# Performance work log

Measured on AMD Instinct MI355X. Metric: run time of the kernel, lower is better.

Reference implementation:

```python
import jax, jax.numpy as jnp
import numpy as np

H, KVH, D, BS, L = 32, 8, 128, 16, 4096
MAX_BLOCKS = L // BS          # 256 blocks per sequence (sink cache capacity)
B = 16
NUM_BLOCKS = B * MAX_BLOCKS   # 4096 total cache blocks
T = MAX_BLOCKS * BS           # 4096 linearized cache slots per sequence
SCALE = 1.0 / np.sqrt(D)


def _rope_cos_sin(pos):
    # neox-style RoPE tables; pos: int array [...]. returns cos/sin [..., D/2]
    inv_freq = 1.0 / (10000.0 ** (jnp.arange(0, D, 2, dtype=jnp.float32) / D))
    ang = pos[..., None].astype(jnp.float32) * inv_freq
    return jnp.cos(ang), jnp.sin(ang)


def _apply_rope(x, cos, sin):
    # x [..., D]; cos/sin broadcastable to x[..., :D//2]
    x1, x2 = jnp.split(x, 2, axis=-1)
    return jnp.concatenate([x1 * cos - x2 * sin, x2 * cos + x1 * sin], axis=-1)


def setup_inputs() -> dict:
    key = jax.random.key(0)
    ks = jax.random.split(key, 6)
    q = jax.random.normal(ks[0], (B, H * D), dtype=jnp.float32)
    k = jax.random.normal(ks[1], (B, KVH * D), dtype=jnp.float32)
    v = jax.random.normal(ks[2], (B, KVH * D), dtype=jnp.float32)
    key_cache = jax.random.normal(ks[3], (NUM_BLOCKS, BS, KVH, D), dtype=jnp.float32)
    value_cache = jax.random.normal(ks[4], (NUM_BLOCKS, BS, KVH, D), dtype=jnp.float32)
    block_tables = jnp.arange(B * MAX_BLOCKS, dtype=jnp.int32).reshape(B, MAX_BLOCKS)
    context_lens = jax.random.randint(ks[5], (B,), 0, 6000, dtype=jnp.int32)
    return {"q": q, "k": k, "v": v, "key_cache": key_cache,
            "value_cache": value_cache, "block_tables": block_tables,
            "context_lens": context_lens}


def reference(q, k, v, key_cache, value_cache, block_tables, context_lens):
    ctx = context_lens.astype(jnp.int32)                         # [B] past tokens
    rem = ctx % BS
    # sink/rolling cap: if past >= model_context_len, effective seq len caps
    seq_len = jnp.where(ctx >= L, L - BS + rem + 1, ctx + 1)     # [B]
    pos_q = seq_len - 1                                          # capped current position

    # gather pre-rope keys/values from paged cache -> [B, T, KVH, D]
    keys = key_cache[block_tables].reshape(B, T, KVH, D)
    vals = value_cache[block_tables].reshape(B, T, KVH, D)

    # re-apply rope to gathered keys at their cache-relative positions 0..T-1
    cos_k, sin_k = _rope_cos_sin(jnp.arange(T))                  # [T, D/2]
    keys = _apply_rope(keys, cos_k[None, :, None, :], sin_k[None, :, None, :])

    # rope current q, k at capped positions
    cos_q, sin_q = _rope_cos_sin(pos_q)                          # [B, D/2]
    qh = _apply_rope(q.reshape(B, H, D), cos_q[:, None, :], sin_q[:, None, :])
    kh = _apply_rope(k.reshape(B, KVH, D), cos_q[:, None, :], sin_q[:, None, :])

    # scatter current token's k/v at its slot (offset rem in last used block == seq_len-1)
    bidx = jnp.arange(B)
    keys = keys.at[bidx, pos_q].set(kh)
    vals = vals.at[bidx, pos_q].set(v.reshape(B, KVH, D))

    # GQA attention over first seq_len cached tokens
    G = H // KVH
    qg = qh.reshape(B, KVH, G, D)
    scores = jnp.einsum('bhgd,bthd->bhgt', qg, keys) * SCALE     # [B, KVH, G, T]
    mask = jnp.arange(T)[None, :] < seq_len[:, None]             # [B, T]
    scores = jnp.where(mask[:, None, None, :], scores, jnp.finfo(scores.dtype).min)
    probs = jax.nn.softmax(scores, axis=-1)
    out = jnp.einsum('bhgt,bthd->bhgd', probs, vals)             # [B, KVH, G, D]
    return out.reshape(B, H * D)
```

## Files before the change

kernel.cpp:

```cpp
#include <hip/hip_runtime.h>
#include <math.h>

#define B_      16
#define H_      32
#define KVH_    8
#define G_      4
#define D_      128
#define BS_     16
#define L_      4096
#define MAXB_   256
#define T_      4096
#define NPART_  16
#define PART_   256
#define SCALE_  0.08838834764831843f

__device__ __forceinline__ int seq_len_of(int ctx) {
  return (ctx >= L_) ? (L_ - BS_ + (ctx & (BS_ - 1)) + 1) : (ctx + 1);
}

__global__ void rope_table_kernel(float* __restrict__ tab) {
  int idx = blockIdx.x * blockDim.x + threadIdx.x;
  if (idx >= T_ * 64) return;
  int t = idx >> 6, i = idx & 63;
  double inv = pow(10000.0, -(double)(2 * i) / 128.0);
  float ang = (float)t * (float)inv;
  double a = (double)ang;
  tab[2 * idx]     = (float)cos(a);
  tab[2 * idx + 1] = (float)sin(a);
}


#define LOADK(P, tt)                                                        \
  {                                                                         \
    int blk_  = sblk[((tt) - t0) >> 4];                                     \
    int base_ = ((blk_ * BS_ + ((tt) & (BS_ - 1))) * KVH_ + kvh) * D_;      \
    const float4* kc4_ = (const float4*)(kc + base_);                       \
    const float4* vc4_ = (const float4*)(vc + base_);                       \
    P##ka = kc4_[dg];      P##kb = kc4_[16 + dg];                           \
    P##va = vc4_[dg];      P##vb = vc4_[16 + dg];                           \
    P##c0 = tab4[(tt) * 32 + 2 * dg];                                       \
    P##c1 = tab4[(tt) * 32 + 2 * dg + 1];                                   \
  }

#define COMPUTE(P, tt)                                                      \
  {                                                                         \
    float kr1[4], kr2[4];                                                   \
    kr1[0] = P##ka.x * P##c0.x - P##kb.x * P##c0.y;                         \
    kr2[0] = P##kb.x * P##c0.x + P##ka.x * P##c0.y;                         \
    kr1[1] = P##ka.y * P##c0.z - P##kb.y * P##c0.w;                         \
    kr2[1] = P##kb.y * P##c0.z + P##ka.y * P##c0.w;                         \
    kr1[2] = P##ka.z * P##c1.x - P##kb.z * P##c1.y;                         \
    kr2[2] = P##kb.z * P##c1.x + P##ka.z * P##c1.y;                         \
    kr1[3] = P##ka.w * P##c1.z - P##kb.w * P##c1.w;                         \
    kr2[3] = P##kb.w * P##c1.z + P##ka.w * P##c1.w;                         \
    float4 va_ = P##va, vb_ = P##vb;                                        \
    if ((tt) == posq) {         \
      const float* kp_ = knew + b * (KVH_ * D_) + kvh * D_;                 \
      float4 a_  = *(const float4*)(kp_ + 4 * dg);                          \
      float4 b_  = *(const float4*)(kp_ + 64 + 4 * dg);                     \
      float4 q0_ = tab4[posq * 32 + 2 * dg];                                \
      float4 q1_ = tab4[posq * 32 + 2 * dg + 1];                            \
      kr1[0] = a_.x * q0_.x - b_.x * q0_.y;                                 \
      kr2[0] = b_.x * q0_.x + a_.x * q0_.y;                                 \
      kr1[1] = a_.y * q0_.z - b_.y * q0_.w;                                 \
      kr2[1] = b_.y * q0_.z + a_.y * q0_.w;                                 \
      kr1[2] = a_.z * q1_.x - b_.z * q1_.y;                                 \
      kr2[2] = b_.z * q1_.x + a_.z * q1_.y;                                 \
      kr1[3] = a_.w * q1_.z - b_.w * q1_.w;                                 \
      kr2[3] = b_.w * q1_.z + a_.w * q1_.w;                                 \
      const float* vp_ = vnew + b * (KVH_ * D_) + kvh * D_;                 \
      va_ = *(const float4*)(vp_ + 4 * dg);                                 \
      vb_ = *(const float4*)(vp_ + 64 + 4 * dg);                            \
    }                                                                       \
    float s[G_];                                                            \
    _Pragma("unroll")                                                       \
    for (int g = 0; g < G_; ++g) {                                          \
      s[g] = kr1[0] * q1[g][0] + kr2[0] * q2[g][0]                          \
           + kr1[1] * q1[g][1] + kr2[1] * q2[g][1]                          \
           + kr1[2] * q1[g][2] + kr2[2] * q2[g][2]                          \
           + kr1[3] * q1[g][3] + kr2[3] * q2[g][3];                         \
    }                                                                       \
    _Pragma("unroll")                                                       \
    for (int off = 1; off <= 8; off <<= 1) {                                \
      _Pragma("unroll")                                                     \
      for (int g = 0; g < G_; ++g) s[g] += __shfl_xor(s[g], off);           \
    }                                                                       \
    _Pragma("unroll")                                                       \
    for (int g = 0; g < G_; ++g) {                                          \
      float sv = s[g];                                                      \
      float p;                                                              \
      if (sv > m[g]) {                                                      \
        float corr = __expf(m[g] - sv);                                     \
        l[g] *= corr;                                                       \
        _Pragma("unroll")                                                   \
        for (int j = 0; j < 8; ++j) acc[g][j] *= corr;                      \
        m[g] = sv;                                                          \
        p = 1.0f;                                                           \
      } else {                                                              \
        p = __expf(sv - m[g]);                                              \
      }                                                                     \
      l[g] += p;                                                            \
      acc[g][0] += p * va_.x; acc[g][1] += p * va_.y;                       \
      acc[g][2] += p * va_.z; acc[g][3] += p * va_.w;                       \
      acc[g][4] += p * vb_.x; acc[g][5] += p * vb_.y;                       \
      acc[g][6] += p * vb_.z; acc[g][7] += p * vb_.w;                       \
    }                                                                       \
  }

__global__ __launch_bounds__(256) void attn_partial_kernel(
    const float* __restrict__ q, const float* __restrict__ knew,
    const float* __restrict__ vnew, const float* __restrict__ kc,
    const float* __restrict__ vc, const int* __restrict__ btab,
    const int* __restrict__ ctxl, const float* __restrict__ tab,
    float* __restrict__ opart, float2* __restrict__ ml) {
  int bid  = blockIdx.x;
  int part = bid & (NPART_ - 1);
  int kvh  = (bid >> 4) & (KVH_ - 1);
  int b    = bid >> 7;

  int seq = seq_len_of(ctxl[b]);
  int t0 = part * PART_;
  if (t0 >= seq) return;
  int t1 = min(t0 + PART_, seq);
  int posq = seq - 1;

  int lane = threadIdx.x & 63;
  int wave = threadIdx.x >> 6;
  int tsub = lane >> 4;
  int dg   = lane & 15;

  __shared__ int sblk[PART_ / BS_];
  if (threadIdx.x < PART_ / BS_)
    sblk[threadIdx.x] = btab[b * MAXB_ + (t0 >> 4) + threadIdx.x];
  __syncthreads();

  const float4* tab4 = (const float4*)tab;

  float q1[G_][4], q2[G_][4];
  {
    float4 cq0 = tab4[posq * 32 + 2 * dg];
    float4 cq1 = tab4[posq * 32 + 2 * dg + 1];
#pragma unroll
    for (int g = 0; g < G_; ++g) {
      const float* qp = q + b * (H_ * D_) + (kvh * G_ + g) * D_;
      float4 a  = *(const float4*)(qp + 4 * dg);
      float4 bq = *(const float4*)(qp + 64 + 4 * dg);
      q1[g][0] = (a.x * cq0.x - bq.x * cq0.y) * SCALE_;
      q2[g][0] = (bq.x * cq0.x + a.x * cq0.y) * SCALE_;
      q1[g][1] = (a.y * cq0.z - bq.y * cq0.w) * SCALE_;
      q2[g][1] = (bq.y * cq0.z + a.y * cq0.w) * SCALE_;
      q1[g][2] = (a.z * cq1.x - bq.z * cq1.y) * SCALE_;
      q2[g][2] = (bq.z * cq1.x + a.z * cq1.y) * SCALE_;
      q1[g][3] = (a.w * cq1.z - bq.w * cq1.w) * SCALE_;
      q2[g][3] = (bq.w * cq1.z + a.w * cq1.w) * SCALE_;
    }
  }

  float m[G_], l[G_], acc[G_][8];
#pragma unroll
  for (int g = 0; g < G_; ++g) {
    m[g] = -1e30f; l[g] = 0.f;
#pragma unroll
    for (int j = 0; j < 8; ++j) acc[g][j] = 0.f;
  }

  {
    float4 Aka, Akb, Ava, Avb, Ac0, Ac1;
    float4 Bka, Bkb, Bva, Bvb, Bc0, Bc1;
    int t = t0 + 4 * wave + tsub;
    if (t < t1) {
      LOADK(A, t);
      while (1) {
        int t2 = t + 16;
        if (t2 < t1) LOADK(B, t2);
        COMPUTE(A, t);
        t = t2;
        if (t >= t1) break;
        t2 = t + 16;
        if (t2 < t1) LOADK(A, t2);
        COMPUTE(B, t);
        t = t2;
        if (t >= t1) break;
      }
    }
  }

  auto merge_off = [&](int off) {
#pragma unroll
    for (int g = 0; g < G_; ++g) {
      float mo = __shfl_xor(m[g], off);
      float lo = __shfl_xor(l[g], off);
      float M  = fmaxf(m[g], mo);
      float fa = __expf(m[g] - M);
      float fb = __expf(mo - M);
      l[g] = l[g] * fa + lo * fb;
      m[g] = M;
#pragma unroll
      for (int j = 0; j < 8; ++j) {
        float ao = __shfl_xor(acc[g][j], off);
        acc[g][j] = acc[g][j] * fa + ao * fb;
      }
    }
  };
  merge_off(16);
  merge_off(32);

  __shared__ float  lds_acc[4][G_][D_];
  __shared__ float2 lds_ml[4][G_];
  if (lane < 16) {
#pragma unroll
    for (int g = 0; g < G_; ++g) {
#pragma unroll
      for (int j = 0; j < 8; ++j) {
        int dim = (j < 4) ? (4 * dg + j) : (64 + 4 * dg + (j - 4));
        lds_acc[wave][g][dim] = acc[g][j];
      }
      if (lane == 0) lds_ml[wave][g] = make_float2(m[g], l[g]);
    }
  }
  __syncthreads();
  if (wave == 0) {
    int w = tsub;
#pragma unroll
    for (int g = 0; g < G_; ++g) {
      float2 t2 = lds_ml[w][g];
      m[g] = t2.x; l[g] = t2.y;
#pragma unroll
      for (int j = 0; j < 8; ++j) {
        int dim = (j < 4) ? (4 * dg + j) : (64 + 4 * dg + (j - 4));
        acc[g][j] = lds_acc[w][g][dim];
      }
    }
    merge_off(16);
    merge_off(32);
    if (lane < 16) {
#pragma unroll
      for (int g = 0; g < G_; ++g) {
        float* op = opart + (size_t)(bid * G_ + g) * D_;
#pragma unroll
        for (int j = 0; j < 8; ++j) {
          int dim = (j < 4) ? (4 * dg + j) : (64 + 4 * dg + (j - 4));
          op[dim] = acc[g][j];
        }
        if (lane == 0) ml[bid * G_ + g] = make_float2(m[g], l[g]);
      }
    }
  }
}

__global__ void attn_reduce_kernel(const float* __restrict__ opart,
                                   const float2* __restrict__ ml,
                                   const int* __restrict__ ctxl,
                                   float* __restrict__ out) {
  int bh = blockIdx.x;
  int b = bh >> 5, h = bh & 31;
  int kvh = h >> 2, g = h & 3;
  int d = threadIdx.x;
  int seq = seq_len_of(ctxl[b]);
  int nlive = (seq + PART_ - 1) / PART_;
  int base = (b * KVH_ + kvh) * NPART_;

  float M = -1e30f;
  for (int p = 0; p < nlive; ++p) M = fmaxf(M, ml[(base + p) * G_ + g].x);
  float L = 0.f, O = 0.f;
  for (int p = 0; p < nlive; ++p) {
    float2 mlv = ml[(base + p) * G_ + g];
    float f = __expf(mlv.x - M);
    L += mlv.y * f;
    O += opart[(size_t)((base + p) * G_ + g) * D_ + d] * f;
  }
  out[b * (H_ * D_) + h * D_ + d] = O / L;
}

extern "C" void kernel_launch(void* const* d_in, const int* in_sizes, int n_in,
                              void* d_out, int out_size, void* d_ws, size_t ws_size,
                              hipStream_t stream) {
  const float* q    = (const float*)d_in[0];
  const float* k    = (const float*)d_in[1];
  const float* v    = (const float*)d_in[2];
  const float* kc   = (const float*)d_in[3];
  const float* vc   = (const float*)d_in[4];
  const int*   btab = (const int*)d_in[5];
  const int*   ctxl = (const int*)d_in[6];
  float* out = (float*)d_out;

  float*  tab   = (float*)d_ws;
  float*  opart = tab + (size_t)T_ * 64 * 2;
  float2* ml    = (float2*)(opart + (size_t)B_ * KVH_ * NPART_ * G_ * D_);

  rope_table_kernel<<<(T_ * 64 + 255) / 256, 256, 0, stream>>>(tab);
  attn_partial_kernel<<<B_ * KVH_ * NPART_, 256, 0, stream>>>(
      q, k, v, kc, vc, btab, ctxl, tab, opart, ml);
  attn_reduce_kernel<<<B_ * H_, D_, 0, stream>>>(opart, ml, ctxl, out);
}
```

Before: 119.3 us.

## Generate rope cos/sin by rotation recurrence, triple-buffer KV loads, branchless softmax

The per-token cos/sin table loads are replaced by an angle-addition recurrence: each thread loads its starting cos/sin once plus a 16-step rotation and advances by complex multiplication. The online softmax update becomes branchless, always rescaling with fmax and two exps. KV prefetching grows from double to triple buffering so loads are issued two iterations ahead. Together these cut memory traffic on the table and hide more latency, at the cost of extra registers, extra exp work per token, and float drift accumulated across up to 16 recurrence steps.

```diff
diff --git a/kernel.cpp b/kernel.cpp
--- a/kernel.cpp
+++ b/kernel.cpp
@@ -38,36 +38,34 @@
     const float4* vc4_ = (const float4*)(vc + base_);                       \
     P##ka = kc4_[dg];      P##kb = kc4_[16 + dg];                           \
     P##va = vc4_[dg];      P##vb = vc4_[16 + dg];                           \
-    P##c0 = tab4[(tt) * 32 + 2 * dg];                                       \
-    P##c1 = tab4[(tt) * 32 + 2 * dg + 1];                                   \
   }
 
 #define COMPUTE(P, tt)                                                      \
   {                                                                         \
     float kr1[4], kr2[4];                                                   \
-    kr1[0] = P##ka.x * P##c0.x - P##kb.x * P##c0.y;                         \
-    kr2[0] = P##kb.x * P##c0.x + P##ka.x * P##c0.y;                         \
-    kr1[1] = P##ka.y * P##c0.z - P##kb.y * P##c0.w;                         \
-    kr2[1] = P##kb.y * P##c0.z + P##ka.y * P##c0.w;                         \
-    kr1[2] = P##ka.z * P##c1.x - P##kb.z * P##c1.y;                         \
-    kr2[2] = P##kb.z * P##c1.x + P##ka.z * P##c1.y;                         \
-    kr1[3] = P##ka.w * P##c1.z - P##kb.w * P##c1.w;                         \
-    kr2[3] = P##kb.w * P##c1.z + P##ka.w * P##c1.w;                         \
+    kr1[0] = P##ka.x * cc0.x - P##kb.x * cc0.y;                             \
+    kr2[0] = P##kb.x * cc0.x + P##ka.x * cc0.y;                             \
+    kr1[1] = P##ka.y * cc0.z - P##kb.y * cc0.w;                             \
+    kr2[1] = P##kb.y * cc0.z + P##ka.y * cc0.w;                             \
+    kr1[2] = P##ka.z * cc1.x - P##kb.z * cc1.y;                             \
+    kr2[2] = P##kb.z * cc1.x + P##ka.z * cc1.y;                             \
+    kr1[3] = P##ka.w * cc1.z - P##kb.w * cc1.w;                             \
+    kr2[3] = P##kb.w * cc1.z + P##ka.w * cc1.w;                             \
     float4 va_ = P##va, vb_ = P##vb;                                        \
     if ((tt) == posq) {         \
       const float* kp_ = knew + b * (KVH_ * D_) + kvh * D_;                 \
-      float4 a_  = *(const float4*)(kp_ + 4 * dg);                          \
-      float4 b_  = *(const float4*)(kp_ + 64 + 4 * dg);                     \
-      float4 q0_ = tab4[posq * 32 + 2 * dg];                                \
-      float4 q1_ = tab4[posq * 32 + 2 * dg + 1];                            \
-      kr1[0] = a_.x * q0_.x - b_.x * q0_.y;                                 \
-      kr2[0] = b_.x * q0_.x + a_.x * q0_.y;                                 \
-      kr1[1] = a_.y * q0_.z - b_.y * q0_.w;                                 \
-      kr2[1] = b_.y * q0_.z + a_.y * q0_.w;                                 \
-      kr1[2] = a_.z * q1_.x - b_.z * q1_.y;                                 \
-      kr2[2] = b_.z * q1_.x + a_.z * q1_.y;                                 \
-      kr1[3] = a_.w * q1_.z - b_.w * q1_.w;                                 \
-      kr2[3] = b_.w * q1_.z + a_.w * q1_.w;                                 \
+      float4 xa_ = *(const float4*)(kp_ + 4 * dg);                          \
+      float4 xb_ = *(const float4*)(kp_ + 64 + 4 * dg);                     \
+      float4 p0_ = tab4[posq * 32 + 2 * dg];                                \
+      float4 p1_ = tab4[posq * 32 + 2 * dg + 1];                            \
+      kr1[0] = xa_.x * p0_.x - xb_.x * p0_.y;                               \
+      kr2[0] = xb_.x * p0_.x + xa_.x * p0_.y;                               \
+      kr1[1] = xa_.y * p0_.z - xb_.y * p0_.w;                               \
+      kr2[1] = xb_.y * p0_.z + xa_.y * p0_.w;                               \
+      kr1[2] = xa_.z * p1_.x - xb_.z * p1_.y;                               \
+      kr2[2] = xb_.z * p1_.x + xa_.z * p1_.y;                               \
+      kr1[3] = xa_.w * p1_.z - xb_.w * p1_.w;                               \
+      kr2[3] = xb_.w * p1_.z + xa_.w * p1_.w;                               \
       const float* vp_ = vnew + b * (KVH_ * D_) + kvh * D_;                 \
       va_ = *(const float4*)(vp_ + 4 * dg);                                 \
       vb_ = *(const float4*)(vp_ + 64 + 4 * dg);                            \
@@ -87,23 +85,31 @@
     }                                                                       \
     _Pragma("unroll")                                                       \
     for (int g = 0; g < G_; ++g) {                                          \
-      float sv = s[g];                                                      \
-      float p;                                                              \
-      if (sv > m[g]) {                                                      \
-        float corr = __expf(m[g] - sv);                                     \
-        l[g] *= corr;                                                       \
-        _Pragma("unroll")                                                   \
-        for (int j = 0; j < 8; ++j) acc[g][j] *= corr;                      \
-        m[g] = sv;                                                          \
-        p = 1.0f;                                                           \
-      } else {                                                              \
-        p = __expf(sv - m[g]);                                              \
-      }                                                                     \
-      l[g] += p;                                                            \
-      acc[g][0] += p * va_.x; acc[g][1] += p * va_.y;                       \
-      acc[g][2] += p * va_.z; acc[g][3] += p * va_.w;                       \
-      acc[g][4] += p * vb_.x; acc[g][5] += p * vb_.y;                       \
-      acc[g][6] += p * vb_.z; acc[g][7] += p * vb_.w;                       \
+      float sv   = s[g];                                                    \
+      float mn   = fmaxf(m[g], sv);                                         \
+      float corr = __expf(m[g] - mn);                                       \
+      float p    = __expf(sv - mn);                                         \
+      m[g] = mn;                                                            \
+      l[g] = l[g] * corr + p;                                               \
+      acc[g][0] = acc[g][0] * corr + p * va_.x;                             \
+      acc[g][1] = acc[g][1] * corr + p * va_.y;                             \
+      acc[g][2] = acc[g][2] * corr + p * va_.z;                             \
+      acc[g][3] = acc[g][3] * corr + p * va_.w;                             \
+      acc[g][4] = acc[g][4] * corr + p * vb_.x;                             \
+      acc[g][5] = acc[g][5] * corr + p * vb_.y;                             \
+      acc[g][6] = acc[g][6] * corr + p * vb_.z;                             \
+      acc[g][7] = acc[g][7] * corr + p * vb_.w;                             \
+    }                                                                       \
+    {                     \
+      float nc_;                                                            \
+      nc_ = cc0.x * r0.x - cc0.y * r0.y;                                    \
+      cc0.y = cc0.y * r0.x + cc0.x * r0.y; cc0.x = nc_;                     \
+      nc_ = cc0.z * r0.z - cc0.w * r0.w;                                    \
+      cc0.w = cc0.w * r0.z + cc0.z * r0.w; cc0.z = nc_;                     \
+      nc_ = cc1.x * r1.x - cc1.y * r1.y;                                    \
+      cc1.y = cc1.y * r1.x + cc1.x * r1.y; cc1.x = nc_;                     \
+      nc_ = cc1.z * r1.z - cc1.w * r1.w;                                    \
+      cc1.w = cc1.w * r1.z + cc1.z * r1.w; cc1.z = nc_;                     \
     }                                                                       \
   }
 
@@ -135,6 +141,12 @@
   __syncthreads();
 
   const float4* tab4 = (const float4*)tab;
+
+  int tstart = t0 + 4 * wave + tsub;
+  float4 cc0 = tab4[tstart * 32 + 2 * dg];
+  float4 cc1 = tab4[tstart * 32 + 2 * dg + 1];
+  float4 r0  = tab4[16 * 32 + 2 * dg];
+  float4 r1  = tab4[16 * 32 + 2 * dg + 1];
 
   float q1[G_][4], q2[G_][4];
   {
@@ -165,22 +177,23 @@
   }
 
   {
-    float4 Aka, Akb, Ava, Avb, Ac0, Ac1;
-    float4 Bka, Bkb, Bva, Bvb, Bc0, Bc1;
+    float4 Aka, Akb, Ava, Avb;
+    float4 Bka, Bkb, Bva, Bvb;
+    float4 Cka, Ckb, Cva, Cvb;
     int t = t0 + 4 * wave + tsub;
     if (t < t1) {
       LOADK(A, t);
+      if (t + 16 < t1) LOADK(B, t + 16);
       while (1) {
-        int t2 = t + 16;
-        if (t2 < t1) LOADK(B, t2);
+        if (t + 32 < t1) LOADK(C, t + 32);
         COMPUTE(A, t);
-        t = t2;
-        if (t >= t1) break;
-        t2 = t + 16;
-        if (t2 < t1) LOADK(A, t2);
+        t += 16; if (t >= t1) break;
+        if (t + 32 < t1) LOADK(A, t + 32);
         COMPUTE(B, t);
-        t = t2;
-        if (t >= t1) break;
+        t += 16; if (t >= t1) break;
+        if (t + 32 < t1) LOADK(B, t + 32);
+        COMPUTE(C, t);
+        t += 16; if (t >= t1) break;
       }
     }
   }
```

New measurement: 119.1 us. About the same (-0.2%).
